# Kernel tuning notes

Hardware: AMD Instinct MI355X
Metric: run time of the kernel (lower is better)

The kernel has to match this reference:

```python
import jax, jax.numpy as jnp
import numpy as np

_BLOCK = 32          # _QUANTIZATION_BLOCK_SIZE
_UPPER = 8           # upper_bound = 2**(4-1)-1 + 1 for Q4_0 (bitwidth=4)
_QMAX = 15.0         # 2**bitwidth - 1


def _q4_0_dequant(kernel):
    """Vectorized Q4_0 fake-quantization over 32-element blocks (last axis, no transpose)."""
    orig_dtype = kernel.dtype
    nb = kernel.size // _BLOCK
    blocks = kernel.reshape(nb, _BLOCK).astype(jnp.float32)  # [nb, 32]
    # signed value at the abs-argmax position of each block
    amax_idx = jnp.argmax(jnp.abs(blocks), axis=1)
    max_val = jnp.take_along_axis(blocks, amax_idx[:, None], axis=1)  # [nb, 1]
    d = -max_val / _UPPER
    safe_d = jnp.where(d == 0.0, 1.0, d)
    safe_inv_d = jnp.where(d == 0.0, 0.0, 1.0 / safe_d)
    scale = d.astype(jnp.float16).astype(jnp.float32)  # fp16 scale round-trip
    qs = jnp.clip(jnp.trunc(blocks * safe_inv_d + (_UPPER + 0.5)), 0.0, _QMAX)
    deq = scale * (qs - _UPPER)
    return deq.reshape(kernel.shape).astype(orig_dtype)


def _ste_q4_0(kernel):
    """Straight-through estimator wrapper (identity gradient)."""
    zero = kernel - jax.lax.stop_gradient(kernel)
    return zero + jax.lax.stop_gradient(_q4_0_dequant(kernel))


def setup_inputs() -> dict:
    key = jax.random.key(0)
    k1, k2, k3 = jax.random.split(key, 3)
    d_in, features = 8192, 8192
    inputs = jax.random.normal(k1, (1, 32, d_in), dtype=jnp.float32)
    kernel = jax.random.normal(k2, (d_in, features), dtype=jnp.float32) * 0.02
    bias = jax.random.normal(k3, (features,), dtype=jnp.float32) * 0.02
    return {"inputs": inputs, "kernel": kernel, "bias": bias}


def reference(inputs, kernel, bias):
    w = _ste_q4_0(kernel)                      # fake-quantized weight [d_in, features]
    y = inputs @ w                             # [B, S, features]
    y = y + bias
    return y
```

## Files before the change

kernel.cpp:

```cpp
#include <hip/hip_runtime.h>
#include <hip/hip_fp16.h>

#define MDIM 32
#define KDIM 8192
#define NDIM 8192
#define NT 256
#define KC 512
#define BK 32
#define NTILES (KC / BK)

typedef _Float16 half2_t __attribute__((ext_vector_type(2)));

#if __has_builtin(__builtin_amdgcn_fdot2)
__device__ __forceinline__ float fdot2(half2_t a, half2_t b, float c) {
  return __builtin_amdgcn_fdot2(a, b, c, false);
}
#else
__device__ __forceinline__ float fdot2(half2_t a, half2_t b, float c) {
  return c + (float)a.x * (float)b.x + (float)a.y * (float)b.y;
}
#endif

__device__ __forceinline__ half2_t pk_f16(float a, float b) {
#if __has_builtin(__builtin_amdgcn_cvt_pkrtz)
  return __builtin_bit_cast(half2_t, __builtin_amdgcn_cvt_pkrtz(a, b));
#else
  half2_t r; r.x = (_Float16)a; r.y = (_Float16)b; return r;
#endif
}

__global__ __launch_bounds__(256) void fused_q4_gemm(
    const float* __restrict__ x,
    const float* __restrict__ w,
    const float* __restrict__ bias,
    float* __restrict__ out)
{
  __shared__ __align__(16) float2 s_scale[8 * BK];
  __shared__ __align__(16) unsigned int s_x2[(BK / 2) * 36];

  const int t  = threadIdx.x;
  const int n0 = blockIdx.x * NT;
  const int k0 = blockIdx.y * KC;

  const int gn  = n0 + t;
  const int nb2 = t >> 5;

  float acc[MDIM];
#pragma unroll
  for (int m = 0; m < MDIM; ++m) acc[m] = 0.0f;

  const int krow = t >> 3;
  const int nb   = t & 7;

  for (int tt = 0; tt < NTILES; ++tt) {
    const int kt = k0 + tt * BK;

    {
      const float* bp = w + (size_t)(kt + krow) * NDIM + n0 + nb * 32;
      float best_abs = -1.0f, best_val = 0.0f;
#pragma unroll
      for (int j = 0; j < 8; ++j) {
        float4 v = reinterpret_cast<const float4*>(bp)[j];
        float a;
        a = fabsf(v.x); if (a > best_abs) { best_abs = a; best_val = v.x; }
        a = fabsf(v.y); if (a > best_abs) { best_abs = a; best_val = v.y; }
        a = fabsf(v.z); if (a > best_abs) { best_abs = a; best_val = v.z; }
        a = fabsf(v.w); if (a > best_abs) { best_abs = a; best_val = v.w; }
      }
      float d   = best_val * -0.125f;
      float inv = (d == 0.0f) ? 0.0f : 1.0f / d;
      float sc  = __half2float(__float2half(d));
      s_scale[nb * BK + krow] = make_float2(sc, inv);
    }

#pragma unroll
    for (int j = 0; j < 2; ++j) {
      int idx = t + j * 256;
      int kp  = idx & 15;
      int m   = idx >> 4;
      float2 xv = *reinterpret_cast<const float2*>(x + (size_t)m * KDIM + kt + 2 * kp);
      half2_t h = pk_f16(xv.x, xv.y);
      s_x2[kp * 36 + m] = __builtin_bit_cast(unsigned int, h);
    }

    __syncthreads();

    const float* colp = w + (size_t)kt * NDIM + gn;
    const float4* svp = reinterpret_cast<const float4*>(s_scale) + nb2 * (BK / 2);
#pragma unroll
    for (int kp = 0; kp < BK / 2; ++kp) {
      float w0 = colp[(2 * kp) * NDIM];
      float w1 = colp[(2 * kp + 1) * NDIM];
      float4 sv = svp[kp];
      float t0  = fmaf(w0, sv.y, 8.5f);
      float q0  = fminf(fmaxf(truncf(t0), 0.0f), 15.0f);
      float dq0 = (q0 - 8.0f) * sv.x;
      float t1  = fmaf(w1, sv.w, 8.5f);
      float q1  = fminf(fmaxf(truncf(t1), 0.0f), 15.0f);
      float dq1 = (q1 - 8.0f) * sv.z;
      half2_t w2 = pk_f16(dq0, dq1);
      const uint4* xrow = reinterpret_cast<const uint4*>(s_x2 + kp * 36);
#pragma unroll
      for (int g = 0; g < 8; ++g) {
        uint4 xq = xrow[g];
        acc[4 * g + 0] = fdot2(w2, __builtin_bit_cast(half2_t, xq.x), acc[4 * g + 0]);
        acc[4 * g + 1] = fdot2(w2, __builtin_bit_cast(half2_t, xq.y), acc[4 * g + 1]);
        acc[4 * g + 2] = fdot2(w2, __builtin_bit_cast(half2_t, xq.z), acc[4 * g + 2]);
        acc[4 * g + 3] = fdot2(w2, __builtin_bit_cast(half2_t, xq.w), acc[4 * g + 3]);
      }
    }
    __syncthreads();
  }

  const float bv = (blockIdx.y == 0) ? bias[gn] : 0.0f;
#pragma unroll
  for (int m = 0; m < MDIM; ++m) {
    atomicAdd(out + (size_t)m * NDIM + gn, acc[m] + bv);
  }
}

extern "C" void kernel_launch(void* const* d_in, const int* in_sizes, int n_in,
                              void* d_out, int out_size, void* d_ws, size_t ws_size,
                              hipStream_t stream) {
  const float* x    = (const float*)d_in[0];
  const float* w    = (const float*)d_in[1];
  const float* bias = (const float*)d_in[2];
  float* out = (float*)d_out;

  (void)hipMemsetAsync(out, 0, (size_t)MDIM * NDIM * sizeof(float), stream);

  dim3 grid(NDIM / NT, KDIM / KC);
  fused_q4_gemm<<<grid, 256, 0, stream>>>(x, w, bias, out);
}
```

Before: 423.9 us.

## Dequantize weights once into LDS and pre-pack activations in separate kernel

Adds a pre-pass kernel that converts activations to packed fp16 pairs in a workspace laid out k-major. The main kernel now reads each weight element from global memory once, computes block scales with a lane shuffle, and stores dequantized fp16 pairs in padded LDS. Before, each weight was loaded twice: once for the scale and once for the dot product. Each thread now handles 16 of the 32 rows over a 128-column tile, reading activations from the global/L2 workspace instead of LDS. The cost is an extra kernel launch and activation reads that now go through cache rather than shared memory.

```diff
diff --git a/kernel.cpp b/kernel.cpp
--- a/kernel.cpp
+++ b/kernel.cpp
@@ -4,10 +4,11 @@
 #define MDIM 32
 #define KDIM 8192
 #define NDIM 8192
-#define NT 256
+#define NT 128
 #define KC 512
-#define BK 32
+#define BK 64
 #define NTILES (KC / BK)
+#define WPAD 132
 
 typedef _Float16 half2_t __attribute__((ext_vector_type(2)));
 
@@ -21,101 +22,161 @@
 }
 #endif
 
-__device__ __forceinline__ half2_t pk_f16(float a, float b) {
+__device__ __forceinline__ unsigned pk_u32(float a, float b) {
 #if __has_builtin(__builtin_amdgcn_cvt_pkrtz)
-  return __builtin_bit_cast(half2_t, __builtin_amdgcn_cvt_pkrtz(a, b));
+  return __builtin_bit_cast(unsigned, __builtin_amdgcn_cvt_pkrtz(a, b));
 #else
-  half2_t r; r.x = (_Float16)a; r.y = (_Float16)b; return r;
+  half2_t r; r.x = (_Float16)a; r.y = (_Float16)b;
+  return __builtin_bit_cast(unsigned, r);
 #endif
 }
 
-__global__ __launch_bounds__(256) void fused_q4_gemm(
+__device__ __forceinline__ half2_t u2h(unsigned u) {
+  return __builtin_bit_cast(half2_t, u);
+}
+
+__global__ __launch_bounds__(256) void xpack_kernel(const float* __restrict__ x,
+                                                    unsigned* __restrict__ xp) {
+  __shared__ float sx[32][129];
+  const int t  = threadIdx.x;
+  const int k0 = blockIdx.x * 128;
+  {
+    const int m = t >> 3, c = (t & 7) * 16;
+    const float* p = x + (size_t)m * KDIM + k0 + c;
+#pragma unroll
+    for (int j = 0; j < 4; ++j) {
+      float4 v = reinterpret_cast<const float4*>(p)[j];
+      sx[m][c + j * 4 + 0] = v.x;
+      sx[m][c + j * 4 + 1] = v.y;
+      sx[m][c + j * 4 + 2] = v.z;
+      sx[m][c + j * 4 + 3] = v.w;
+    }
+  }
+  __syncthreads();
+  const int kpl = t & 63, mh = t >> 6;
+  unsigned pw[8];
+#pragma unroll
+  for (int j = 0; j < 8; ++j) {
+    int mm = mh * 8 + j;
+    pw[j] = pk_u32(sx[mm][2 * kpl], sx[mm][2 * kpl + 1]);
+  }
+  uint4* dst = reinterpret_cast<uint4*>(xp + ((size_t)(k0 >> 1) + kpl) * 32 + mh * 8);
+  dst[0] = make_uint4(pw[0], pw[1], pw[2], pw[3]);
+  dst[1] = make_uint4(pw[4], pw[5], pw[6], pw[7]);
+}
+
+__global__ __launch_bounds__(256, 4) void fused_q4_gemm(
     const float* __restrict__ x,
+    const unsigned* __restrict__ xp,
     const float* __restrict__ w,
     const float* __restrict__ bias,
     float* __restrict__ out)
 {
-  __shared__ __align__(16) float2 s_scale[8 * BK];
-  __shared__ __align__(16) unsigned int s_x2[(BK / 2) * 36];
+  __shared__ unsigned s_w2[32 * WPAD];
 
   const int t  = threadIdx.x;
   const int n0 = blockIdx.x * NT;
   const int k0 = blockIdx.y * KC;
 
-  const int gn  = n0 + t;
-  const int nb2 = t >> 5;
+  const int kr = t >> 3;
+  const int nc = t & 7;
+  const int n_local = t & 127;
+  const int gn = n0 + n_local;
+  const int mbase = (__builtin_amdgcn_readfirstlane(t) >> 7) << 4;
 
-  float acc[MDIM];
+  float acc[16];
 #pragma unroll
-  for (int m = 0; m < MDIM; ++m) acc[m] = 0.0f;
-
-  const int krow = t >> 3;
-  const int nb   = t & 7;
+  for (int j = 0; j < 16; ++j) acc[j] = 0.0f;
 
   for (int tt = 0; tt < NTILES; ++tt) {
     const int kt = k0 + tt * BK;
 
     {
-      const float* bp = w + (size_t)(kt + krow) * NDIM + n0 + nb * 32;
-      float best_abs = -1.0f, best_val = 0.0f;
+      const float* rp = w + (size_t)(kt + 2 * kr) * NDIM + n0 + nc * 16;
+      float4 v0[4], v1[4];
 #pragma unroll
-      for (int j = 0; j < 8; ++j) {
-        float4 v = reinterpret_cast<const float4*>(bp)[j];
-        float a;
-        a = fabsf(v.x); if (a > best_abs) { best_abs = a; best_val = v.x; }
-        a = fabsf(v.y); if (a > best_abs) { best_abs = a; best_val = v.y; }
-        a = fabsf(v.z); if (a > best_abs) { best_abs = a; best_val = v.z; }
-        a = fabsf(v.w); if (a > best_abs) { best_abs = a; best_val = v.w; }
+      for (int j = 0; j < 4; ++j) {
+        v0[j] = reinterpret_cast<const float4*>(rp)[j];
+        v1[j] = reinterpret_cast<const float4*>(rp + NDIM)[j];
       }
-      float d   = best_val * -0.125f;
-      float inv = (d == 0.0f) ? 0.0f : 1.0f / d;
-      float sc  = __half2float(__float2half(d));
-      s_scale[nb * BK + krow] = make_float2(sc, inv);
-    }
+      float ba0 = -1.0f, bv0 = 0.0f, ba1 = -1.0f, bv1 = 0.0f;
+#pragma unroll
+      for (int j = 0; j < 4; ++j) {
+        float c, a;
+        c = v0[j].x; a = fabsf(c); if (a > ba0) { ba0 = a; bv0 = c; }
+        c = v0[j].y; a = fabsf(c); if (a > ba0) { ba0 = a; bv0 = c; }
+        c = v0[j].z; a = fabsf(c); if (a > ba0) { ba0 = a; bv0 = c; }
+        c = v0[j].w; a = fabsf(c); if (a > ba0) { ba0 = a; bv0 = c; }
+        c = v1[j].x; a = fabsf(c); if (a > ba1) { ba1 = a; bv1 = c; }
+        c = v1[j].y; a = fabsf(c); if (a > ba1) { ba1 = a; bv1 = c; }
+        c = v1[j].z; a = fabsf(c); if (a > ba1) { ba1 = a; bv1 = c; }
+        c = v1[j].w; a = fabsf(c); if (a > ba1) { ba1 = a; bv1 = c; }
+      }
+      float pa0 = __shfl_xor(ba0, 1), pv0 = __shfl_xor(bv0, 1);
+      float pa1 = __shfl_xor(ba1, 1), pv1 = __shfl_xor(bv1, 1);
+      const bool odd = (t & 1);
+      if (odd ? (pa0 >= ba0) : (pa0 > ba0)) bv0 = pv0;
+      if (odd ? (pa1 >= ba1) : (pa1 > ba1)) bv1 = pv1;
 
+      float d0 = bv0 * -0.125f;
+      float i0 = (d0 == 0.0f) ? 0.0f : 1.0f / d0;
+      float s0 = __half2float(__float2half(d0));
+      float d1 = bv1 * -0.125f;
+      float i1 = (d1 == 0.0f) ? 0.0f : 1.0f / d1;
+      float s1 = __half2float(__float2half(d1));
+
+      unsigned pw[16];
 #pragma unroll
-    for (int j = 0; j < 2; ++j) {
-      int idx = t + j * 256;
-      int kp  = idx & 15;
-      int m   = idx >> 4;
-      float2 xv = *reinterpret_cast<const float2*>(x + (size_t)m * KDIM + kt + 2 * kp);
-      half2_t h = pk_f16(xv.x, xv.y);
-      s_x2[kp * 36 + m] = __builtin_bit_cast(unsigned int, h);
+      for (int j = 0; j < 4; ++j) {
+        float q, a0f, a1f;
+#define DQ(comp, idx)                                                      \
+        q = fminf(fmaxf(truncf(fmaf(v0[j].comp, i0, 8.5f)), 0.0f), 15.0f); \
+        a0f = (q - 8.0f) * s0;                                             \
+        q = fminf(fmaxf(truncf(fmaf(v1[j].comp, i1, 8.5f)), 0.0f), 15.0f); \
+        a1f = (q - 8.0f) * s1;                                             \
+        pw[j * 4 + idx] = pk_u32(a0f, a1f);
+        DQ(x, 0) DQ(y, 1) DQ(z, 2) DQ(w, 3)
+#undef DQ
+      }
+      uint4* wp = reinterpret_cast<uint4*>(&s_w2[kr * WPAD + nc * 16]);
+      wp[0] = make_uint4(pw[0],  pw[1],  pw[2],  pw[3]);
+      wp[1] = make_uint4(pw[4],  pw[5],  pw[6],  pw[7]);
+      wp[2] = make_uint4(pw[8],  pw[9],  pw[10], pw[11]);
+      wp[3] = make_uint4(pw[12], pw[13], pw[14], pw[15]);
     }
 
     __syncthreads();
 
-    const float* colp = w + (size_t)kt * NDIM + gn;
-    const float4* svp = reinterpret_cast<const float4*>(s_scale) + nb2 * (BK / 2);
-#pragma unroll
+    const int kb = kt >> 1;
+#pragma unroll 4
     for (int kp = 0; kp < BK / 2; ++kp) {
-      float w0 = colp[(2 * kp) * NDIM];
-      float w1 = colp[(2 * kp + 1) * NDIM];
-      float4 sv = svp[kp];
-      float t0  = fmaf(w0, sv.y, 8.5f);
-      float q0  = fminf(fmaxf(truncf(t0), 0.0f), 15.0f);
-      float dq0 = (q0 - 8.0f) * sv.x;
-      float t1  = fmaf(w1, sv.w, 8.5f);
-      float q1  = fminf(fmaxf(truncf(t1), 0.0f), 15.0f);
-      float dq1 = (q1 - 8.0f) * sv.z;
-      half2_t w2 = pk_f16(dq0, dq1);
-      const uint4* xrow = reinterpret_cast<const uint4*>(s_x2 + kp * 36);
-#pragma unroll
-      for (int g = 0; g < 8; ++g) {
-        uint4 xq = xrow[g];
-        acc[4 * g + 0] = fdot2(w2, __builtin_bit_cast(half2_t, xq.x), acc[4 * g + 0]);
-        acc[4 * g + 1] = fdot2(w2, __builtin_bit_cast(half2_t, xq.y), acc[4 * g + 1]);
-        acc[4 * g + 2] = fdot2(w2, __builtin_bit_cast(half2_t, xq.z), acc[4 * g + 2]);
-        acc[4 * g + 3] = fdot2(w2, __builtin_bit_cast(half2_t, xq.w), acc[4 * g + 3]);
-      }
+      half2_t w2 = u2h(s_w2[kp * WPAD + n_local]);
+      const uint4* xr = reinterpret_cast<const uint4*>(xp + (size_t)(kb + kp) * 32 + mbase);
+      uint4 q0 = xr[0], q1 = xr[1], q2 = xr[2], q3 = xr[3];
+      acc[0]  = fdot2(w2, u2h(q0.x), acc[0]);
+      acc[1]  = fdot2(w2, u2h(q0.y), acc[1]);
+      acc[2]  = fdot2(w2, u2h(q0.z), acc[2]);
+      acc[3]  = fdot2(w2, u2h(q0.w), acc[3]);
+      acc[4]  = fdot2(w2, u2h(q1.x), acc[4]);
+      acc[5]  = fdot2(w2, u2h(q1.y), acc[5]);
+      acc[6]  = fdot2(w2, u2h(q1.z), acc[6]);
+      acc[7]  = fdot2(w2, u2h(q1.w), acc[7]);
+      acc[8]  = fdot2(w2, u2h(q2.x), acc[8]);
+      acc[9]  = fdot2(w2, u2h(q2.y), acc[9]);
+      acc[10] = fdot2(w2, u2h(q2.z), acc[10]);
+      acc[11] = fdot2(w2, u2h(q2.w), acc[11]);
+      acc[12] = fdot2(w2, u2h(q3.x), acc[12]);
+      acc[13] = fdot2(w2, u2h(q3.y), acc[13]);
+      acc[14] = fdot2(w2, u2h(q3.z), acc[14]);
+      acc[15] = fdot2(w2, u2h(q3.w), acc[15]);
     }
     __syncthreads();
   }
 
   const float bv = (blockIdx.y == 0) ? bias[gn] : 0.0f;
 #pragma unroll
-  for (int m = 0; m < MDIM; ++m) {
-    atomicAdd(out + (size_t)m * NDIM + gn, acc[m] + bv);
+  for (int j = 0; j < 16; ++j) {
+    atomicAdd(out + (size_t)(mbase + j) * NDIM + gn, acc[j] + bv);
   }
 }
 
@@ -125,10 +186,12 @@
   const float* x    = (const float*)d_in[0];
   const float* w    = (const float*)d_in[1];
   const float* bias = (const float*)d_in[2];
-  float* out = (float*)d_out;
+  float* out  = (float*)d_out;
+  unsigned* xp = (unsigned*)d_ws;
 
   (void)hipMemsetAsync(out, 0, (size_t)MDIM * NDIM * sizeof(float), stream);
+  xpack_kernel<<<64, 256, 0, stream>>>(x, xp);
 
   dim3 grid(NDIM / NT, KDIM / KC);
-  fused_q4_gemm<<<grid, 256, 0, stream>>>(x, w, bias, out);
+  fused_q4_gemm<<<grid, 256, 0, stream>>>(x, xp, w, bias, out);
 }
```

Result: faster. 372.4 us (-12.2%).
